# Kernel tuning notes

Hardware: AMD Instinct MI355X
Metric: run time of the kernel (lower is better)

The kernel has to match this reference:

```python
import jax, jax.numpy as jnp
import numpy as np

N = 50000


def gcn_conv(x, W, b, src, dst, deg_inv_sqrt):
    # h = x @ W, then symmetric-normalized aggregation with self-loops
    h = x @ W  # [N, out]
    norm = deg_inv_sqrt[src] * deg_inv_sqrt[dst]  # [E]
    agg = jax.ops.segment_sum(h[src] * norm[:, None], dst, num_segments=N)
    # self-loop contribution: norm_ii = deg_inv_sqrt[i]^2
    agg = agg + h * (deg_inv_sqrt * deg_inv_sqrt)[:, None]
    return agg + b


def setup_inputs() -> dict:
    key = jax.random.key(0)
    ks = jax.random.split(key, 8)
    F_in, H, C = 128, 128, 64
    x = jax.random.normal(ks[0], (N, F_in), dtype=jnp.float32)
    edge_index = jax.random.randint(ks[1], (2, 800000), 0, N, dtype=jnp.int64)
    s = 1.0 / np.sqrt(F_in)
    W1 = jax.random.uniform(ks[2], (F_in, H), jnp.float32, -s, s)
    b1 = jnp.zeros((H,), jnp.float32)
    W2 = jax.random.uniform(ks[3], (H, H), jnp.float32, -s, s)
    b2 = jnp.zeros((H,), jnp.float32)
    W3 = jax.random.uniform(ks[4], (H, C), jnp.float32, -s, s)
    b3 = jnp.zeros((C,), jnp.float32)
    return {"x": x, "edge_index": edge_index, "W1": W1, "b1": b1,
            "W2": W2, "b2": b2, "W3": W3, "b3": b3}


def reference(x, edge_index, W1, b1, W2, b2, W3, b3):
    src, dst = edge_index[0], edge_index[1]
    # degree with self-loops (edge weight 1): deg[i] = in-degree + 1
    deg = jnp.zeros((N,), x.dtype).at[dst].add(1.0) + 1.0
    dinv = jax.lax.rsqrt(deg)
    h = gcn_conv(x, W1, b1, src, dst, dinv)
    h = jax.nn.relu(h)  # dropout p=0 / eval -> identity
    h = gcn_conv(h, W2, b2, src, dst, dinv)
    h = jax.nn.relu(h)
    h = gcn_conv(h, W3, b3, src, dst, dinv)
    return jax.nn.log_softmax(h, axis=-1)
```

## Files before the change

### kernel.cpp

```cpp
#include <hip/hip_runtime.h>
#include <math.h>

typedef short short8 __attribute__((ext_vector_type(8)));
typedef float floatx4 __attribute__((ext_vector_type(4)));

__device__ __forceinline__ float4 ld4(const float* p) { return *reinterpret_cast<const float4*>(p); }
__device__ __forceinline__ void st4(float* p, float4 v) { *reinterpret_cast<float4*>(p) = v; }

__device__ __forceinline__ float bf2f(unsigned int u) { return __uint_as_float(u << 16); }
__device__ __forceinline__ unsigned int f2bf1(float f) {
    unsigned int x = __float_as_uint(f);
    return (x + 0x7fffu + ((x >> 16) & 1u)) >> 16;
}
__device__ __forceinline__ unsigned int f2bf2(float lo, float hi) {
    return f2bf1(lo) | (f2bf1(hi) << 16);
}
__device__ __forceinline__ void unpack8(uint4 v, float* f) {
    f[0] = bf2f(v.x & 0xffffu); f[1] = bf2f(v.x >> 16);
    f[2] = bf2f(v.y & 0xffffu); f[3] = bf2f(v.y >> 16);
    f[4] = bf2f(v.z & 0xffffu); f[5] = bf2f(v.z >> 16);
    f[6] = bf2f(v.w & 0xffffu); f[7] = bf2f(v.w >> 16);
}

__global__ __launch_bounds__(256) void k_count(const int* __restrict__ dst, int* __restrict__ deg,
                                               int* __restrict__ rank, int E) {
    int e = blockIdx.x * 256 + threadIdx.x;
    if (e < E) rank[e] = atomicAdd(&deg[dst[e]], 1);
}

__global__ __launch_bounds__(256) void k_reduce256(const int* __restrict__ deg, int* __restrict__ bsum, int n) {
    __shared__ int s[256];
    int t = threadIdx.x;
    int i = blockIdx.x * 256 + t;
    s[t] = (i < n) ? deg[i] : 0;
    __syncthreads();
    for (int off = 128; off > 0; off >>= 1) {
        if (t < off) s[t] += s[t + off];
        __syncthreads();
    }
    if (t == 0) bsum[blockIdx.x] = s[0];
}

__global__ __launch_bounds__(256) void k_scan_small(const int* __restrict__ bsum, int* __restrict__ boff, int nb) {
    __shared__ int s[256];
    int t = threadIdx.x;
    int v = (t < nb) ? bsum[t] : 0;
    s[t] = v;
    __syncthreads();
    for (int off = 1; off < 256; off <<= 1) {
        int x = (t >= off) ? s[t - off] : 0;
        __syncthreads();
        s[t] += x;
        __syncthreads();
    }
    if (t < nb) boff[t] = s[t] - v;
}

__global__ __launch_bounds__(256) void k_scan_final(const int* __restrict__ deg, const int* __restrict__ boff,
                                                    int* __restrict__ row_off, float* __restrict__ dinv, int n) {
    __shared__ int s[256];
    int t = threadIdx.x;
    int i = blockIdx.x * 256 + t;
    int v = (i < n) ? deg[i] : 0;
    s[t] = v;
    __syncthreads();
    for (int off = 1; off < 256; off <<= 1) {
        int x = (t >= off) ? s[t - off] : 0;
        __syncthreads();
        s[t] += x;
        __syncthreads();
    }
    int incl = s[t] + boff[blockIdx.x];
    if (i < n) {
        row_off[i] = incl - v;
        dinv[i]    = 1.0f / sqrtf((float)v + 1.0f);
        if (i == n - 1) row_off[n] = incl;
    }
}

__global__ __launch_bounds__(256) void k_fill(const int* __restrict__ src, const int* __restrict__ dst,
                                              const int* __restrict__ rank, const int* __restrict__ roff,
                                              const float* __restrict__ dinv, int2* __restrict__ cpair, int E) {
    int e = blockIdx.x * 256 + threadIdx.x;
    if (e < E) {
        int s = src[e], d = dst[e];
        int pos = roff[d] + rank[e];
        cpair[pos] = make_int2(s, __float_as_int(dinv[s] * dinv[d]));
    }
}

__global__ __launch_bounds__(256) void k_prepW(const float* __restrict__ W1, const float* __restrict__ W2,
                                               const float* __restrict__ W3, unsigned short* __restrict__ Wt1,
                                               unsigned short* __restrict__ Wt2, unsigned short* __restrict__ Wt3) {
    int t = blockIdx.x * 256 + threadIdx.x;
    if (t < 16384) {
        int k = t & 127, n = t >> 7;
        Wt1[n * 128 + k] = (unsigned short)f2bf1(W1[(size_t)k * 128 + n]);
    } else if (t < 32768) {
        int u = t - 16384;
        int k = u & 127, n = u >> 7;
        Wt2[n * 128 + k] = (unsigned short)f2bf1(W2[(size_t)k * 128 + n]);
    } else if (t < 40960) {
        int u = t - 32768;
        int k = u & 127, n = u >> 7;
        Wt3[n * 128 + k] = (unsigned short)f2bf1(W3[(size_t)k * 64 + n]);
    }
}

template <int NC, bool XF32>
__global__ __launch_bounds__(256) void k_gemm_mfma(const void* __restrict__ Xv, const unsigned short* __restrict__ Wt,
                                                   unsigned short* __restrict__ O, int nrows) {
    constexpr int LDR = 136;
    __shared__ unsigned short sX[64 * LDR];
    __shared__ unsigned short sB[NC * LDR];

    const int tid  = threadIdx.x;
    const int row0 = blockIdx.x * 64;

    if constexpr (XF32) {
        const float* X = (const float*)Xv;
#pragma unroll
        for (int i = 0; i < 4; ++i) {
            int idx = tid + i * 256;
            int r = idx >> 4, c8 = idx & 15;
            int grow = row0 + r;
            uint4 v = make_uint4(0, 0, 0, 0);
            if (grow < nrows) {
                float4 a = ld4(X + (size_t)grow * 128 + c8 * 8);
                float4 b = ld4(X + (size_t)grow * 128 + c8 * 8 + 4);
                v = make_uint4(f2bf2(a.x, a.y), f2bf2(a.z, a.w), f2bf2(b.x, b.y), f2bf2(b.z, b.w));
            }
            *reinterpret_cast<uint4*>(&sX[r * LDR + c8 * 8]) = v;
        }
    } else {
        const unsigned short* X = (const unsigned short*)Xv;
#pragma unroll
        for (int i = 0; i < 4; ++i) {
            int idx = tid + i * 256;
            int r = idx >> 4, c8 = idx & 15;
            int grow = row0 + r;
            uint4 v = make_uint4(0, 0, 0, 0);
            if (grow < nrows) v = *reinterpret_cast<const uint4*>(X + (size_t)grow * 128 + c8 * 8);
            *reinterpret_cast<uint4*>(&sX[r * LDR + c8 * 8]) = v;
        }
    }
#pragma unroll
    for (int i = 0; i < NC / 16; ++i) {
        int idx = tid + i * 256;
        int n = idx >> 4, c8 = idx & 15;
        *reinterpret_cast<uint4*>(&sB[n * LDR + c8 * 8]) =
            *reinterpret_cast<const uint4*>(Wt + (size_t)n * 128 + c8 * 8);
    }
    __syncthreads();

    const int lane = tid & 63;
    const int wave = tid >> 6;
    const int l15  = lane & 15;
    const int quad = lane >> 4;

    floatx4 acc[NC / 16];
#pragma unroll
    for (int j = 0; j < NC / 16; ++j) acc[j] = (floatx4){0.f, 0.f, 0.f, 0.f};

    const unsigned short* xbase = &sX[(wave * 16 + l15) * LDR + quad * 8];
#pragma unroll
    for (int kk = 0; kk < 4; ++kk) {
        short8 xb = *reinterpret_cast<const short8*>(xbase + kk * 32);
#pragma unroll
        for (int j = 0; j < NC / 16; ++j) {
            short8 wa = *reinterpret_cast<const short8*>(&sB[(j * 16 + l15) * LDR + quad * 8 + kk * 32]);
            acc[j] = __builtin_amdgcn_mfma_f32_16x16x32_bf16(wa, xb, acc[j], 0, 0, 0);
        }
    }

    int xrow = row0 + wave * 16 + l15;
    if (xrow < nrows) {
#pragma unroll
        for (int j = 0; j < NC / 16; ++j) {
            uint2 o = make_uint2(f2bf2(acc[j][0], acc[j][1]), f2bf2(acc[j][2], acc[j][3]));
            *reinterpret_cast<uint2*>(O + (size_t)xrow * NC + j * 16 + quad * 4) = o;
        }
    }
}

__global__ __launch_bounds__(256) void k_agg_relu(const unsigned short* __restrict__ H, const int* __restrict__ roff,
                                                  const int2* __restrict__ cpair, const float* __restrict__ dinv,
                                                  const float* __restrict__ bias, unsigned short* __restrict__ O, int n) {
    int t    = blockIdx.x * 256 + threadIdx.x;
    int node = t >> 4;
    int f8   = (t & 15) * 8;
    if (node >= n) return;

    float di = dinv[node];
    float sc = di * di;
    float a[8];
    {
        uint4 hv = *reinterpret_cast<const uint4*>(H + (size_t)node * 128 + f8);
        float h[8];
        unpack8(hv, h);
#pragma unroll
        for (int i = 0; i < 8; ++i) a[i] = h[i] * sc;
    }

    int e  = roff[node];
    int e1 = roff[node + 1];
    for (; e + 7 < e1; e += 8) {
        int2 pr[8];
        uint4 v[8];
#pragma unroll
        for (int u = 0; u < 8; ++u) pr[u] = cpair[e + u];
#pragma unroll
        for (int u = 0; u < 8; ++u) v[u] = *reinterpret_cast<const uint4*>(H + (size_t)pr[u].x * 128 + f8);
#pragma unroll
        for (int u = 0; u < 8; ++u) {
            float nu = __int_as_float(pr[u].y);
            float gg[8];
            unpack8(v[u], gg);
#pragma unroll
            for (int i = 0; i < 8; ++i) a[i] += gg[i] * nu;
        }
    }
    if (e + 3 < e1) {
        int2 pr[4];
        uint4 v[4];
#pragma unroll
        for (int u = 0; u < 4; ++u) pr[u] = cpair[e + u];
#pragma unroll
        for (int u = 0; u < 4; ++u) v[u] = *reinterpret_cast<const uint4*>(H + (size_t)pr[u].x * 128 + f8);
#pragma unroll
        for (int u = 0; u < 4; ++u) {
            float nu = __int_as_float(pr[u].y);
            float gg[8];
            unpack8(v[u], gg);
#pragma unroll
            for (int i = 0; i < 8; ++i) a[i] += gg[i] * nu;
        }
        e += 4;
    }
    for (; e < e1; ++e) {
        int2 p0 = cpair[e];
        float n0 = __int_as_float(p0.y);
        uint4 v0 = *reinterpret_cast<const uint4*>(H + (size_t)p0.x * 128 + f8);
        float g0[8];
        unpack8(v0, g0);
#pragma unroll
        for (int i = 0; i < 8; ++i) a[i] += g0[i] * n0;
    }

    float4 b0 = ld4(bias + f8);
    float4 b1 = ld4(bias + f8 + 4);
    float bb[8] = {b0.x, b0.y, b0.z, b0.w, b1.x, b1.y, b1.z, b1.w};
#pragma unroll
    for (int i = 0; i < 8; ++i) a[i] = fmaxf(a[i] + bb[i], 0.0f);

    uint4 ov = make_uint4(f2bf2(a[0], a[1]), f2bf2(a[2], a[3]), f2bf2(a[4], a[5]), f2bf2(a[6], a[7]));
    *reinterpret_cast<uint4*>(O + (size_t)node * 128 + f8) = ov;
}

__global__ __launch_bounds__(256) void k_agg_softmax(const unsigned short* __restrict__ H, const int* __restrict__ roff,
                                                     const int2* __restrict__ cpair, const float* __restrict__ dinv,
                                                     const float* __restrict__ bias, float* __restrict__ O, int n) {
    int t    = blockIdx.x * 256 + threadIdx.x;
    int node = t >> 3;
    int f8   = (t & 7) * 8;
    if (node >= n) return;

    float di = dinv[node];
    float sc = di * di;
    float a[8];
    {
        uint4 hv = *reinterpret_cast<const uint4*>(H + (size_t)node * 64 + f8);
        float h[8];
        unpack8(hv, h);
#pragma unroll
        for (int i = 0; i < 8; ++i) a[i] = h[i] * sc;
    }

    int e  = roff[node];
    int e1 = roff[node + 1];
    for (; e + 7 < e1; e += 8) {
        int2 pr[8];
        uint4 v[8];
#pragma unroll
        for (int u = 0; u < 8; ++u) pr[u] = cpair[e + u];
#pragma unroll
        for (int u = 0; u < 8; ++u) v[u] = *reinterpret_cast<const uint4*>(H + (size_t)pr[u].x * 64 + f8);
#pragma unroll
        for (int u = 0; u < 8; ++u) {
            float nu = __int_as_float(pr[u].y);
            float gg[8];
            unpack8(v[u], gg);
#pragma unroll
            for (int i = 0; i < 8; ++i) a[i] += gg[i] * nu;
        }
    }
    if (e + 3 < e1) {
        int2 pr[4];
        uint4 v[4];
#pragma unroll
        for (int u = 0; u < 4; ++u) pr[u] = cpair[e + u];
#pragma unroll
        for (int u = 0; u < 4; ++u) v[u] = *reinterpret_cast<const uint4*>(H + (size_t)pr[u].x * 64 + f8);
#pragma unroll
        for (int u = 0; u < 4; ++u) {
            float nu = __int_as_float(pr[u].y);
            float gg[8];
            unpack8(v[u], gg);
#pragma unroll
            for (int i = 0; i < 8; ++i) a[i] += gg[i] * nu;
        }
        e += 4;
    }
    for (; e < e1; ++e) {
        int2 p0 = cpair[e];
        float n0 = __int_as_float(p0.y);
        uint4 v0 = *reinterpret_cast<const uint4*>(H + (size_t)p0.x * 64 + f8);
        float g0[8];
        unpack8(v0, g0);
#pragma unroll
        for (int i = 0; i < 8; ++i) a[i] += g0[i] * n0;
    }

    float4 b0 = ld4(bias + f8);
    float4 b1 = ld4(bias + f8 + 4);
    float bb[8] = {b0.x, b0.y, b0.z, b0.w, b1.x, b1.y, b1.z, b1.w};
    float v[8];
#pragma unroll
    for (int i = 0; i < 8; ++i) v[i] = a[i] + bb[i];

    float m = v[0];
#pragma unroll
    for (int i = 1; i < 8; ++i) m = fmaxf(m, v[i]);
    m = fmaxf(m, __shfl_xor(m, 1));
    m = fmaxf(m, __shfl_xor(m, 2));
    m = fmaxf(m, __shfl_xor(m, 4));

    float ssum = 0.0f;
#pragma unroll
    for (int i = 0; i < 8; ++i) ssum += expf(v[i] - m);
    ssum += __shfl_xor(ssum, 1);
    ssum += __shfl_xor(ssum, 2);
    ssum += __shfl_xor(ssum, 4);
    float ls = logf(ssum);

    float* op = O + (size_t)node * 64 + f8;
    st4(op, make_float4(v[0] - m - ls, v[1] - m - ls, v[2] - m - ls, v[3] - m - ls));
    st4(op + 4, make_float4(v[4] - m - ls, v[5] - m - ls, v[6] - m - ls, v[7] - m - ls));
}

extern "C" void kernel_launch(void* const* d_in, const int* in_sizes, int n_in,
                              void* d_out, int out_size, void* d_ws, size_t ws_size,
                              hipStream_t stream) {
    const float* x  = (const float*)d_in[0];
    const int*   ei = (const int*)d_in[1];
    const float* W1 = (const float*)d_in[2];
    const float* b1 = (const float*)d_in[3];
    const float* W2 = (const float*)d_in[4];
    const float* b2 = (const float*)d_in[5];
    const float* W3 = (const float*)d_in[6];
    const float* b3 = (const float*)d_in[7];
    float* out = (float*)d_out;

    const int N = in_sizes[0] / 128;
    const int E = in_sizes[1] / 2;
    const int* src = ei;
    const int* dst = ei + E;

    char* ws = (char*)d_ws;
    size_t off = 0;
    auto alloc = [&](size_t bytes) -> char* {
        char* p = ws + off;
        off = (off + bytes + 255) & ~(size_t)255;
        return p;
    };
    int nb = (N + 255) / 256;
    int*   deg     = (int*)alloc((size_t)N * 4);
    int*   row_off = (int*)alloc(((size_t)N + 1) * 4);
    float* dinv    = (float*)alloc((size_t)N * 4);
    int*   bsum    = (int*)alloc((size_t)nb * 4);
    int*   boff    = (int*)alloc((size_t)nb * 4);
    int*   rank    = (int*)alloc((size_t)E * 4);
    int2*  cpair   = (int2*)alloc((size_t)E * 8);
    unsigned short* Wt1  = (unsigned short*)alloc(128 * 128 * 2);
    unsigned short* Wt2  = (unsigned short*)alloc(128 * 128 * 2);
    unsigned short* Wt3  = (unsigned short*)alloc(64 * 128 * 2);
    unsigned short* bufA = (unsigned short*)alloc((size_t)N * 128 * 2);
    unsigned short* bufB = (unsigned short*)alloc((size_t)N * 128 * 2);
    unsigned short* bufC = (unsigned short*)alloc((size_t)N * 64 * 2);
    (void)ws_size; (void)n_in; (void)out_size;

    hipMemsetAsync(deg, 0, (size_t)N * 4, stream);
    k_count<<<(E + 255) / 256, 256, 0, stream>>>(dst, deg, rank, E);
    k_reduce256<<<nb, 256, 0, stream>>>(deg, bsum, N);
    k_scan_small<<<1, 256, 0, stream>>>(bsum, boff, nb);
    k_scan_final<<<nb, 256, 0, stream>>>(deg, boff, row_off, dinv, N);
    k_fill<<<(E + 255) / 256, 256, 0, stream>>>(src, dst, rank, row_off, dinv, cpair, E);

    k_prepW<<<(40960 + 255) / 256, 256, 0, stream>>>(W1, W2, W3, Wt1, Wt2, Wt3);

    int blocks64 = (N + 63) / 64;
    k_gemm_mfma<128, true><<<blocks64, 256, 0, stream>>>(x, Wt1, bufA, N);
    k_agg_relu<<<((size_t)N * 16 + 255) / 256, 256, 0, stream>>>(bufA, row_off, cpair, dinv, b1, bufB, N);
    k_gemm_mfma<128, false><<<blocks64, 256, 0, stream>>>(bufB, Wt2, bufA, N);
    k_agg_relu<<<((size_t)N * 16 + 255) / 256, 256, 0, stream>>>(bufA, row_off, cpair, dinv, b2, bufB, N);
    k_gemm_mfma<64, false><<<blocks64, 256, 0, stream>>>(bufB, Wt3, bufC, N);
    k_agg_softmax<<<((size_t)N * 8 + 255) / 256, 256, 0, stream>>>(bufC, row_off, cpair, dinv, b3, out, N);
}
```

Measured before the change: 269.2 us.

## Merge independent setup kernels and gemm1 into shared launches, trim agg unroll

Merges the edge-count kernel with weight transposition/bf16 conversion into one launch, and the degree block-reduce with the first layer GEMM into another, using blockIdx ranges to split roles. This removes kernel launches and lets independent work overlap on the GPU. The aggregation inner loop drops from 8-way to 4-way unrolling, which lowers register pressure but exposes fewer concurrent gathers. The merged gemm block shares an oversized LDS allocation with the reduce blocks, which may limit occupancy for those blocks.

```diff
diff --git a/kernel.cpp b/kernel.cpp
--- a/kernel.cpp
+++ b/kernel.cpp
@@ -22,23 +22,105 @@
     f[6] = bf2f(v.w & 0xffffu); f[7] = bf2f(v.w >> 16);
 }
 
-__global__ __launch_bounds__(256) void k_count(const int* __restrict__ dst, int* __restrict__ deg,
-                                               int* __restrict__ rank, int E) {
-    int e = blockIdx.x * 256 + threadIdx.x;
-    if (e < E) rank[e] = atomicAdd(&deg[dst[e]], 1);
-}
-
-__global__ __launch_bounds__(256) void k_reduce256(const int* __restrict__ deg, int* __restrict__ bsum, int n) {
-    __shared__ int s[256];
-    int t = threadIdx.x;
-    int i = blockIdx.x * 256 + t;
-    s[t] = (i < n) ? deg[i] : 0;
+__global__ __launch_bounds__(256) void k_count_prep(const int* __restrict__ dst, int* __restrict__ deg,
+                                                    int* __restrict__ rank, int E, int nbE,
+                                                    const float* __restrict__ W1, const float* __restrict__ W2,
+                                                    const float* __restrict__ W3, unsigned short* __restrict__ Wt1,
+                                                    unsigned short* __restrict__ Wt2, unsigned short* __restrict__ Wt3) {
+    if ((int)blockIdx.x < nbE) {
+        int e = blockIdx.x * 256 + threadIdx.x;
+        if (e < E) rank[e] = atomicAdd(&deg[dst[e]], 1);
+    } else {
+        int t = (blockIdx.x - nbE) * 256 + threadIdx.x;
+        if (t < 16384) {
+            int k = t & 127, n = t >> 7;
+            Wt1[n * 128 + k] = (unsigned short)f2bf1(W1[(size_t)k * 128 + n]);
+        } else if (t < 32768) {
+            int u = t - 16384;
+            int k = u & 127, n = u >> 7;
+            Wt2[n * 128 + k] = (unsigned short)f2bf1(W2[(size_t)k * 128 + n]);
+        } else if (t < 40960) {
+            int u = t - 32768;
+            int k = u & 127, n = u >> 7;
+            Wt3[n * 128 + k] = (unsigned short)f2bf1(W3[(size_t)k * 64 + n]);
+        }
+    }
+}
+
+__global__ __launch_bounds__(256) void k_reduce_gemm1(const int* __restrict__ deg, int* __restrict__ bsum, int n, int nb,
+                                                      const float* __restrict__ X, const unsigned short* __restrict__ Wt,
+                                                      unsigned short* __restrict__ O, int nrows) {
+    constexpr int LDR = 136;
+    __shared__ __align__(16) unsigned char smem[(64 * LDR + 128 * LDR) * 2];
+
+    const int tid = threadIdx.x;
+    if ((int)blockIdx.x < nb) {
+        int* s = (int*)smem;
+        int i = blockIdx.x * 256 + tid;
+        s[tid] = (i < n) ? deg[i] : 0;
+        __syncthreads();
+        for (int off = 128; off > 0; off >>= 1) {
+            if (tid < off) s[tid] += s[tid + off];
+            __syncthreads();
+        }
+        if (tid == 0) bsum[blockIdx.x] = s[0];
+        return;
+    }
+
+    unsigned short* sX = (unsigned short*)smem;
+    unsigned short* sB = sX + 64 * LDR;
+    const int row0 = (blockIdx.x - nb) * 64;
+
+#pragma unroll
+    for (int i = 0; i < 4; ++i) {
+        int idx = tid + i * 256;
+        int r = idx >> 4, c8 = idx & 15;
+        int grow = row0 + r;
+        uint4 v = make_uint4(0, 0, 0, 0);
+        if (grow < nrows) {
+            float4 a = ld4(X + (size_t)grow * 128 + c8 * 8);
+            float4 b = ld4(X + (size_t)grow * 128 + c8 * 8 + 4);
+            v = make_uint4(f2bf2(a.x, a.y), f2bf2(a.z, a.w), f2bf2(b.x, b.y), f2bf2(b.z, b.w));
+        }
+        *reinterpret_cast<uint4*>(&sX[r * LDR + c8 * 8]) = v;
+    }
+#pragma unroll
+    for (int i = 0; i < 8; ++i) {
+        int idx = tid + i * 256;
+        int nn = idx >> 4, c8 = idx & 15;
+        *reinterpret_cast<uint4*>(&sB[nn * LDR + c8 * 8]) =
+            *reinterpret_cast<const uint4*>(Wt + (size_t)nn * 128 + c8 * 8);
+    }
     __syncthreads();
-    for (int off = 128; off > 0; off >>= 1) {
-        if (t < off) s[t] += s[t + off];
-        __syncthreads();
-    }
-    if (t == 0) bsum[blockIdx.x] = s[0];
+
+    const int lane = tid & 63;
+    const int wave = tid >> 6;
+    const int l15  = lane & 15;
+    const int quad = lane >> 4;
+
+    floatx4 acc[8];
+#pragma unroll
+    for (int j = 0; j < 8; ++j) acc[j] = (floatx4){0.f, 0.f, 0.f, 0.f};
+
+    const unsigned short* xbase = &sX[(wave * 16 + l15) * LDR + quad * 8];
+#pragma unroll
+    for (int kk = 0; kk < 4; ++kk) {
+        short8 xb = *reinterpret_cast<const short8*>(xbase + kk * 32);
+#pragma unroll
+        for (int j = 0; j < 8; ++j) {
+            short8 wa = *reinterpret_cast<const short8*>(&sB[(j * 16 + l15) * LDR + quad * 8 + kk * 32]);
+            acc[j] = __builtin_amdgcn_mfma_f32_16x16x32_bf16(wa, xb, acc[j], 0, 0, 0);
+        }
+    }
+
+    int xrow = row0 + wave * 16 + l15;
+    if (xrow < nrows) {
+#pragma unroll
+        for (int j = 0; j < 8; ++j) {
+            uint2 o = make_uint2(f2bf2(acc[j][0], acc[j][1]), f2bf2(acc[j][2], acc[j][3]));
+            *reinterpret_cast<uint2*>(O + (size_t)xrow * 128 + j * 16 + quad * 4) = o;
+        }
+    }
 }
 
 __global__ __launch_bounds__(256) void k_scan_small(const int* __restrict__ bsum, int* __restrict__ boff, int nb) {
@@ -89,26 +171,9 @@
     }
 }
 
-__global__ __launch_bounds__(256) void k_prepW(const float* __restrict__ W1, const float* __restrict__ W2,
-                                               const float* __restrict__ W3, unsigned short* __restrict__ Wt1,
-                                               unsigned short* __restrict__ Wt2, unsigned short* __restrict__ Wt3) {
-    int t = blockIdx.x * 256 + threadIdx.x;
-    if (t < 16384) {
-        int k = t & 127, n = t >> 7;
-        Wt1[n * 128 + k] = (unsigned short)f2bf1(W1[(size_t)k * 128 + n]);
-    } else if (t < 32768) {
-        int u = t - 16384;
-        int k = u & 127, n = u >> 7;
-        Wt2[n * 128 + k] = (unsigned short)f2bf1(W2[(size_t)k * 128 + n]);
-    } else if (t < 40960) {
-        int u = t - 32768;
-        int k = u & 127, n = u >> 7;
-        Wt3[n * 128 + k] = (unsigned short)f2bf1(W3[(size_t)k * 64 + n]);
-    }
-}
-
-template <int NC, bool XF32>
-__global__ __launch_bounds__(256) void k_gemm_mfma(const void* __restrict__ Xv, const unsigned short* __restrict__ Wt,
+template <int NC>
+__global__ __launch_bounds__(256) void k_gemm_mfma(const unsigned short* __restrict__ X,
+                                                   const unsigned short* __restrict__ Wt,
                                                    unsigned short* __restrict__ O, int nrows) {
     constexpr int LDR = 136;
     __shared__ unsigned short sX[64 * LDR];
@@ -117,32 +182,14 @@
     const int tid  = threadIdx.x;
     const int row0 = blockIdx.x * 64;
 
-    if constexpr (XF32) {
-        const float* X = (const float*)Xv;
-#pragma unroll
-        for (int i = 0; i < 4; ++i) {
-            int idx = tid + i * 256;
-            int r = idx >> 4, c8 = idx & 15;
-            int grow = row0 + r;
-            uint4 v = make_uint4(0, 0, 0, 0);
-            if (grow < nrows) {
-                float4 a = ld4(X + (size_t)grow * 128 + c8 * 8);
-                float4 b = ld4(X + (size_t)grow * 128 + c8 * 8 + 4);
-                v = make_uint4(f2bf2(a.x, a.y), f2bf2(a.z, a.w), f2bf2(b.x, b.y), f2bf2(b.z, b.w));
-            }
-            *reinterpret_cast<uint4*>(&sX[r * LDR + c8 * 8]) = v;
-        }
-    } else {
-        const unsigned short* X = (const unsigned short*)Xv;
-#pragma unroll
-        for (int i = 0; i < 4; ++i) {
-            int idx = tid + i * 256;
-            int r = idx >> 4, c8 = idx & 15;
-            int grow = row0 + r;
-            uint4 v = make_uint4(0, 0, 0, 0);
-            if (grow < nrows) v = *reinterpret_cast<const uint4*>(X + (size_t)grow * 128 + c8 * 8);
-            *reinterpret_cast<uint4*>(&sX[r * LDR + c8 * 8]) = v;
-        }
+#pragma unroll
+    for (int i = 0; i < 4; ++i) {
+        int idx = tid + i * 256;
+        int r = idx >> 4, c8 = idx & 15;
+        int grow = row0 + r;
+        uint4 v = make_uint4(0, 0, 0, 0);
+        if (grow < nrows) v = *reinterpret_cast<const uint4*>(X + (size_t)grow * 128 + c8 * 8);
+        *reinterpret_cast<uint4*>(&sX[r * LDR + c8 * 8]) = v;
     }
 #pragma unroll
     for (int i = 0; i < NC / 16; ++i) {
@@ -204,38 +251,21 @@
 
     int e  = roff[node];
     int e1 = roff[node + 1];
-    for (; e + 7 < e1; e += 8) {
-        int2 pr[8];
-        uint4 v[8];
-#pragma unroll
-        for (int u = 0; u < 8; ++u) pr[u] = cpair[e + u];
-#pragma unroll
-        for (int u = 0; u < 8; ++u) v[u] = *reinterpret_cast<const uint4*>(H + (size_t)pr[u].x * 128 + f8);
-#pragma unroll
-        for (int u = 0; u < 8; ++u) {
-            float nu = __int_as_float(pr[u].y);
-            float gg[8];
-            unpack8(v[u], gg);
-#pragma unroll
-            for (int i = 0; i < 8; ++i) a[i] += gg[i] * nu;
-        }
-    }
-    if (e + 3 < e1) {
-        int2 pr[4];
+    for (; e + 3 < e1; e += 4) {
+        int2 p[4];
         uint4 v[4];
 #pragma unroll
-        for (int u = 0; u < 4; ++u) pr[u] = cpair[e + u];
-#pragma unroll
-        for (int u = 0; u < 4; ++u) v[u] = *reinterpret_cast<const uint4*>(H + (size_t)pr[u].x * 128 + f8);
+        for (int u = 0; u < 4; ++u) p[u] = cpair[e + u];
+#pragma unroll
+        for (int u = 0; u < 4; ++u) v[u] = *reinterpret_cast<const uint4*>(H + (size_t)p[u].x * 128 + f8);
 #pragma unroll
         for (int u = 0; u < 4; ++u) {
-            float nu = __int_as_float(pr[u].y);
-            float gg[8];
-            unpack8(v[u], gg);
-#pragma unroll
-            for (int i = 0; i < 8; ++i) a[i] += gg[i] * nu;
-        }
-        e += 4;
+            float nu = __int_as_float(p[u].y);
+            float g[8];
+            unpack8(v[u], g);
+#pragma unroll
+            for (int i = 0; i < 8; ++i) a[i] += g[i] * nu;
+        }
     }
     for (; e < e1; ++e) {
         int2 p0 = cpair[e];
@@ -373,7 +403,10 @@
         off = (off + bytes + 255) & ~(size_t)255;
         return p;
     };
-    int nb = (N + 255) / 256;
+    int nb  = (N + 255) / 256;
+    int nbE = (E + 255) / 256;
+    int blocks64 = (N + 63) / 64;
+
     int*   deg     = (int*)alloc((size_t)N * 4);
     int*   row_off = (int*)alloc(((size_t)N + 1) * 4);
     float* dinv    = (float*)alloc((size_t)N * 4);
@@ -390,19 +423,15 @@
     (void)ws_size; (void)n_in; (void)out_size;
 
     hipMemsetAsync(deg, 0, (size_t)N * 4, stream);
-    k_count<<<(E + 255) / 256, 256, 0, stream>>>(dst, deg, rank, E);
-    k_reduce256<<<nb, 256, 0, stream>>>(deg, bsum, N);
+    k_count_prep<<<nbE + 160, 256, 0, stream>>>(dst, deg, rank, E, nbE, W1, W2, W3, Wt1, Wt2, Wt3);
+    k_reduce_gemm1<<<nb + blocks64, 256, 0, stream>>>(deg, bsum, N, nb, x, Wt1, bufA, N);
     k_scan_small<<<1, 256, 0, stream>>>(bsum, boff, nb);
     k_scan_final<<<nb, 256, 0, stream>>>(deg, boff, row_off, dinv, N);
-    k_fill<<<(E + 255) / 256, 256, 0, stream>>>(src, dst, rank, row_off, dinv, cpair, E);
-
-    k_prepW<<<(40960 + 255) / 256, 256, 0, stream>>>(W1, W2, W3, Wt1, Wt2, Wt3);
-
-    int blocks64 = (N + 63) / 64;
-    k_gemm_mfma<128, true><<<blocks64, 256, 0, stream>>>(x, Wt1, bufA, N);
+    k_fill<<<nbE, 256, 0, stream>>>(src, dst, rank, row_off, dinv, cpair, E);
+
     k_agg_relu<<<((size_t)N * 16 + 255) / 256, 256, 0, stream>>>(bufA, row_off, cpair, dinv, b1, bufB, N);
-    k_gemm_mfma<128, false><<<blocks64, 256, 0, stream>>>(bufB, Wt2, bufA, N);
+    k_gemm_mfma<128><<<blocks64, 256, 0, stream>>>(bufB, Wt2, bufA, N);
     k_agg_relu<<<((size_t)N * 16 + 255) / 256, 256, 0, stream>>>(bufA, row_off, cpair, dinv, b2, bufB, N);
-    k_gemm_mfma<64, false><<<blocks64, 256, 0, stream>>>(bufB, Wt3, bufC, N);
+    k_gemm_mfma<64><<<blocks64, 256, 0, stream>>>(bufB, Wt3, bufC, N);
     k_agg_softmax<<<((size_t)N * 8 + 255) / 256, 256, 0, stream>>>(bufC, row_off, cpair, dinv, b3, out, N);
 }
```

Measured after the change: 256.3 us. 4.8% less time.
